# Kernel optimization log

Measured on AMD Instinct MI355X. Metric: run time of the kernel, lower is better.

Reference implementation:

```python
import jax, jax.numpy as jnp
import numpy as np

NUM_HEADS = 16


def setup_inputs() -> dict:
    key = jax.random.key(0)
    ks = jax.random.split(key, 6)
    B, N, M, C = 2, 2048, 2048, 1024
    return {
        "reference_data": jax.random.normal(ks[0], (B, N, C), dtype=jnp.float32),
        "target_data": jax.random.normal(ks[1], (B, M, C), dtype=jnp.float32),
        "Wq": jax.random.normal(ks[2], (C, C), dtype=jnp.float32) * (C ** -0.5),
        "Wkv": jax.random.normal(ks[3], (C, 2 * C), dtype=jnp.float32) * (C ** -0.5),
        "Wproj": jax.random.normal(ks[4], (C, C), dtype=jnp.float32) * (C ** -0.5),
        "bproj": jnp.zeros((C,), dtype=jnp.float32),
    }


def reference(reference_data, target_data, Wq, Wkv, Wproj, bproj):
    B, N, C = reference_data.shape
    M = target_data.shape[1]
    H = NUM_HEADS
    hd = C // H
    scale = hd ** -0.5
    # k, v from reference: [B, N, 2, H, hd] -> two [B, H, N, hd]
    kv = (reference_data @ Wkv).reshape(B, N, 2, H, hd)
    k = jnp.transpose(kv[:, :, 0], (0, 2, 1, 3))  # [B,H,N,hd]
    v = jnp.transpose(kv[:, :, 1], (0, 2, 1, 3))  # [B,H,N,hd]
    # q from target: [B, H, M, hd]
    q = jnp.transpose((target_data @ Wq).reshape(B, M, H, hd), (0, 2, 1, 3))
    attn = jnp.einsum("bhid,bhjd->bhij", q, k) * scale  # [B,H,M,N]
    attn = jax.nn.softmax(attn, axis=-1)
    x = jnp.einsum("bhij,bhjd->bhid", attn, v)  # [B,H,M,hd]
    x = jnp.transpose(x, (0, 2, 1, 3)).reshape(B, M, C)
    return x @ Wproj + bproj
```

## Files before the change

### kernel.cpp

```cpp
#include <hip/hip_runtime.h>
#include <hip/hip_bf16.h>
#include <stdint.h>

#define SEQ   2048
#define CH    1024
#define NH    16
#define HD    64

typedef short bf8 __attribute__((ext_vector_type(8)));
typedef short bf4 __attribute__((ext_vector_type(4)));
typedef float f4  __attribute__((ext_vector_type(4)));
typedef unsigned short u16;

#define GAS(p) ((const __attribute__((address_space(1))) void*)(p))
#define LAS(p) ((__attribute__((address_space(3))) void*)(p))

__device__ __forceinline__ u16 f2bf(float f) {
  uint32_t u = __float_as_uint(f);
  u += 0x7fffu + ((u >> 16) & 1u);
  return (u16)(u >> 16);
}

__device__ __forceinline__ uint32_t pk2bf(float a, float b) {
  float2 f; f.x = a; f.y = b;
  __hip_bfloat162 h = __float22bfloat162_rn(f);
  union { __hip_bfloat162 h; uint32_t u; } cv; cv.h = h;
  return cv.u;
}

__device__ __forceinline__ f4 MFMA32(bf8 a, bf8 b, f4 c) {
  return __builtin_amdgcn_mfma_f32_16x16x32_bf16(a, b, c, 0, 0, 0);
}

__device__ __forceinline__ f4 MFMA16(bf4 a, bf4 b, f4 c) {
#if __has_builtin(__builtin_amdgcn_mfma_f32_16x16x16_bf16)
  return __builtin_amdgcn_mfma_f32_16x16x16_bf16(a, b, c, 0, 0, 0);
#elif __has_builtin(__builtin_amdgcn_mfma_f32_16x16x16bf16_1k)
  return __builtin_amdgcn_mfma_f32_16x16x16bf16_1k(a, b, c, 0, 0, 0);
#else
  f4 d = c;
  asm volatile("v_mfma_f32_16x16x16_bf16 %0, %1, %2, %0"
               : "+v"(d) : "v"(a), "v"(b));
  return d;
#endif
}

__global__ void cvt2_bf16(const float* __restrict__ a, u16* __restrict__ oa,
                          const float* __restrict__ b, u16* __restrict__ ob) {
  int blk = blockIdx.x;
  const float* in; u16* out;
  if (blk < 4096) { in = a; out = oa; } else { in = b; out = ob; blk -= 4096; }
  int i = (blk * 256 + threadIdx.x) * 4;
  float4 f = *reinterpret_cast<const float4*>(in + i);
  ushort4 o;
  o.x = f2bf(f.x); o.y = f2bf(f.y); o.z = f2bf(f.z); o.w = f2bf(f.w);
  *reinterpret_cast<ushort4*>(out + i) = o;
}

__global__ void transp_all(const float* __restrict__ Wq, u16* __restrict__ Wqt,
                           const float* __restrict__ Wkv, u16* __restrict__ Wkvt,
                           const float* __restrict__ Wp, u16* __restrict__ Wpt) {
  __shared__ float tile[32][33];
  int x = blockIdx.x;
  const float* in; u16* out; int N;
  if (x < 32)       { in = Wq;  out = Wqt;  N = CH;     }
  else if (x < 96)  { in = Wkv; out = Wkvt; N = 2 * CH; x -= 32; }
  else              { in = Wp;  out = Wpt;  N = CH;     x -= 96; }
  const int K = CH;
  int bn = x * 32, bk = blockIdx.y * 32;
  int tx = threadIdx.x, ty = threadIdx.y;
  #pragma unroll
  for (int i = ty; i < 32; i += 8)
    tile[i][tx] = in[(size_t)(bk + i) * N + bn + tx];
  __syncthreads();
  #pragma unroll
  for (int i = ty; i < 32; i += 8)
    out[(size_t)(bn + i) * K + bk + tx] = f2bf(tile[tx][i]);
}

__global__ __launch_bounds__(256, 2)
void gemm_qkv(const u16* __restrict__ tgtb, const u16* __restrict__ refb,
              const u16* __restrict__ Wqt, const u16* __restrict__ Wkvt,
              u16* __restrict__ qb, u16* __restrict__ karr, u16* __restrict__ varr)
{
  __shared__ __align__(16) u16 As[128 * 32];
  __shared__ __align__(16) u16 Bs[128 * 32];
  const int tid = threadIdx.x;
  const int lane = tid & 63, wave = tid >> 6;
  const int l16 = lane & 15, q = lane >> 4;
  const bool isQ = blockIdx.x >= 16;
  const u16* A  = isQ ? tgtb : refb;
  const u16* Bt = isQ ? Wqt : Wkvt;
  const int n0 = (isQ ? (blockIdx.x - 16) : blockIdx.x) * 128;
  const int m0 = blockIdx.y * 128;
  const int wm = (wave >> 1) * 64, wn = (wave & 1) * 64;
  const int Kdim = CH;

  f4 acc[4][4] = {};

  for (int k0 = 0; k0 < Kdim; k0 += 32) {
    __syncthreads();
    {
      const int c = tid, c2 = tid + 256;
      __builtin_amdgcn_global_load_lds(
          GAS(&A[(size_t)(m0 + (c >> 2)) * Kdim + k0 + ((c & 3) << 3)]),
          LAS(&As[c << 3]), 16, 0, 0);
      __builtin_amdgcn_global_load_lds(
          GAS(&A[(size_t)(m0 + (c2 >> 2)) * Kdim + k0 + ((c2 & 3) << 3)]),
          LAS(&As[c2 << 3]), 16, 0, 0);
      __builtin_amdgcn_global_load_lds(
          GAS(&Bt[(size_t)(n0 + (c >> 2)) * Kdim + k0 + ((c & 3) << 3)]),
          LAS(&Bs[c << 3]), 16, 0, 0);
      __builtin_amdgcn_global_load_lds(
          GAS(&Bt[(size_t)(n0 + (c2 >> 2)) * Kdim + k0 + ((c2 & 3) << 3)]),
          LAS(&Bs[c2 << 3]), 16, 0, 0);
    }
    __syncthreads();
    bf8 a[4], b[4];
    #pragma unroll
    for (int i = 0; i < 4; ++i)
      a[i] = *reinterpret_cast<const bf8*>(&As[(wm + i * 16 + l16) * 32 + q * 8]);
    #pragma unroll
    for (int j = 0; j < 4; ++j)
      b[j] = *reinterpret_cast<const bf8*>(&Bs[(wn + j * 16 + l16) * 32 + q * 8]);
    #pragma unroll
    for (int i = 0; i < 4; ++i)
      #pragma unroll
      for (int j = 0; j < 4; ++j)
        acc[i][j] = MFMA32(a[i], b[j], acc[i][j]);
  }

  #pragma unroll
  for (int i = 0; i < 4; ++i) {
    const int mbase = m0 + wm + i * 16 + q * 4;
    #pragma unroll
    for (int j = 0; j < 4; ++j) {
      const int n = n0 + wn + j * 16 + l16;
      #pragma unroll
      for (int r = 0; r < 4; ++r) {
        const int m = mbase + r;
        float v = acc[i][j][r];
        if (isQ) {
          int b = m >> 11, ms = m & (SEQ - 1), h = n >> 6, d = n & 63;
          qb[(size_t)((b * NH + h) * SEQ + ms) * HD + d] = f2bf(v * 0.1803368801f);
        } else {
          int b = m >> 11, ns = m & (SEQ - 1);
          if (n < CH) {
            int h = n >> 6, d = n & 63;
            size_t base = (size_t)(b * NH + h) * SEQ * HD;
            int off = (((ns >> 4) * 2 + (d >> 5)) * 4 + ((d >> 3) & 3)) * 128
                      + (ns & 15) * 8 + (d & 7);
            karr[base + off] = f2bf(v);
          } else {
            int c2 = n - CH, h = c2 >> 6, d = c2 & 63;
            size_t base = (size_t)(b * NH + h) * SEQ * HD;
            int off = (((ns >> 4) * 4 + (d >> 4)) * 4 + ((ns >> 2) & 3)) * 64
                      + (d & 15) * 4 + (ns & 3);
            varr[base + off] = f2bf(v);
          }
        }
      }
    }
  }
}

__global__ __launch_bounds__(256, 2)
void gemm_proj(const u16* __restrict__ A, const u16* __restrict__ Bt,
               float* __restrict__ fo, const float* __restrict__ bias)
{
  __shared__ __align__(16) u16 As[128 * 32];
  __shared__ __align__(16) u16 Bs[128 * 32];
  const int tid = threadIdx.x;
  const int lane = tid & 63, wave = tid >> 6;
  const int l16 = lane & 15, q = lane >> 4;
  const int m0 = blockIdx.y * 128, n0 = blockIdx.x * 128;
  const int wm = (wave >> 1) * 64, wn = (wave & 1) * 64;
  const int Kdim = CH;

  f4 acc[4][4] = {};

  for (int k0 = 0; k0 < Kdim; k0 += 32) {
    __syncthreads();
    {
      const int c = tid, c2 = tid + 256;
      __builtin_amdgcn_global_load_lds(
          GAS(&A[(size_t)(m0 + (c >> 2)) * Kdim + k0 + ((c & 3) << 3)]),
          LAS(&As[c << 3]), 16, 0, 0);
      __builtin_amdgcn_global_load_lds(
          GAS(&A[(size_t)(m0 + (c2 >> 2)) * Kdim + k0 + ((c2 & 3) << 3)]),
          LAS(&As[c2 << 3]), 16, 0, 0);
      __builtin_amdgcn_global_load_lds(
          GAS(&Bt[(size_t)(n0 + (c >> 2)) * Kdim + k0 + ((c & 3) << 3)]),
          LAS(&Bs[c << 3]), 16, 0, 0);
      __builtin_amdgcn_global_load_lds(
          GAS(&Bt[(size_t)(n0 + (c2 >> 2)) * Kdim + k0 + ((c2 & 3) << 3)]),
          LAS(&Bs[c2 << 3]), 16, 0, 0);
    }
    __syncthreads();
    bf8 a[4], b[4];
    #pragma unroll
    for (int i = 0; i < 4; ++i)
      a[i] = *reinterpret_cast<const bf8*>(&As[(wm + i * 16 + l16) * 32 + q * 8]);
    #pragma unroll
    for (int j = 0; j < 4; ++j)
      b[j] = *reinterpret_cast<const bf8*>(&Bs[(wn + j * 16 + l16) * 32 + q * 8]);
    #pragma unroll
    for (int i = 0; i < 4; ++i)
      #pragma unroll
      for (int j = 0; j < 4; ++j)
        acc[i][j] = MFMA32(a[i], b[j], acc[i][j]);
  }

  #pragma unroll
  for (int i = 0; i < 4; ++i) {
    const int mbase = m0 + wm + i * 16 + q * 4;
    #pragma unroll
    for (int j = 0; j < 4; ++j) {
      const int n = n0 + wn + j * 16 + l16;
      #pragma unroll
      for (int r = 0; r < 4; ++r)
        fo[(size_t)(mbase + r) * CH + n] = acc[i][j][r] + bias[n];
    }
  }
}

__global__ __launch_bounds__(512, 4)
void attn(const u16* __restrict__ Q, const u16* __restrict__ Karr,
          const u16* __restrict__ Varr, u16* __restrict__ X)
{
  __shared__ __align__(16) u16 Ks[8192];
  __shared__ __align__(16) u16 Vs[8192];
  const int tid = threadIdx.x;
  const int lane = tid & 63, wave = tid >> 6;
  const int l16 = lane & 15, q = lane >> 4;
  const int bh = blockIdx.y;
  const int m0 = blockIdx.x * 128;
  const int wm = wave * 16;

  const u16* Qb = Q    + (size_t)bh * SEQ * HD;
  const u16* Kb = Karr + (size_t)bh * SEQ * HD;
  const u16* Vb = Varr + (size_t)bh * SEQ * HD;

  bf8 qf[2];
  #pragma unroll
  for (int ks = 0; ks < 2; ++ks)
    qf[ks] = *reinterpret_cast<const bf8*>(
        &Qb[(size_t)(m0 + wm + l16) * HD + ks * 32 + q * 8]);

  f4 o[4] = {};
  f4 lsum = {};

  for (int nt = 0; nt < SEQ; nt += 128) {
    __syncthreads();
    {
      const u16* kg = Kb + (size_t)(nt >> 4) * 1024;
      const u16* vg = Vb + (size_t)(nt >> 4) * 1024;
      #pragma unroll
      for (int s = 0; s < 2; ++s) {
        int c = tid + s * 512;
        __builtin_amdgcn_global_load_lds(GAS(kg + c * 8), LAS(Ks + c * 8), 16, 0, 0);
        __builtin_amdgcn_global_load_lds(GAS(vg + c * 8), LAS(Vs + c * 8), 16, 0, 0);
      }
    }
    __syncthreads();

    bf4 pa[8];
    #pragma unroll
    for (int j = 0; j < 8; ++j) {
      bf8 kf0 = *reinterpret_cast<const bf8*>(&Ks[((j * 2 + 0) * 4 + q) * 128 + l16 * 8]);
      bf8 kf1 = *reinterpret_cast<const bf8*>(&Ks[((j * 2 + 1) * 4 + q) * 128 + l16 * 8]);
      f4 z = {};
      z = MFMA32(kf0, qf[0], z);
      z = MFMA32(kf1, qf[1], z);
      f4 p;
      #pragma unroll
      for (int r = 0; r < 4; ++r) p[r] = exp2f(z[r]);
      lsum += p;
      union { bf4 v; uint32_t u[2]; } w;
      w.u[0] = pk2bf(p[0], p[1]);
      w.u[1] = pk2bf(p[2], p[3]);
      pa[j] = w.v;
    }

    #pragma unroll
    for (int j = 0; j < 8; ++j)
      #pragma unroll
      for (int dt = 0; dt < 4; ++dt) {
        bf4 vf = *reinterpret_cast<const bf4*>(&Vs[((j * 4 + dt) * 4 + q) * 64 + l16 * 4]);
        o[dt] = MFMA16(pa[j], vf, o[dt]);
      }
  }

  float ls = lsum[0] + lsum[1] + lsum[2] + lsum[3];
  ls += __shfl_xor(ls, 16);
  ls += __shfl_xor(ls, 32);
  float inv = 1.0f / ls;

  const int b = bh >> 4, h = bh & (NH - 1);
  #pragma unroll
  for (int r = 0; r < 4; ++r) {
    float ir = __shfl(inv, q * 4 + r);
    int m = m0 + wm + q * 4 + r;
    #pragma unroll
    for (int dt = 0; dt < 4; ++dt) {
      int d = dt * 16 + l16;
      X[(size_t)(b * SEQ + m) * CH + h * HD + d] = f2bf(o[dt][r] * ir);
    }
  }
}

extern "C" void kernel_launch(void* const* d_in, const int* in_sizes, int n_in,
                              void* d_out, int out_size, void* d_ws, size_t ws_size,
                              hipStream_t stream) {
  const float* ref   = (const float*)d_in[0];
  const float* tgt   = (const float*)d_in[1];
  const float* Wq    = (const float*)d_in[2];
  const float* Wkv   = (const float*)d_in[3];
  const float* Wproj = (const float*)d_in[4];
  const float* bproj = (const float*)d_in[5];
  float* out = (float*)d_out;

  char* ws = (char*)d_ws;
  u16* refb = (u16*)(ws);
  u16* tgtb = (u16*)(ws + (8  << 20));
  u16* Wqt  = (u16*)(ws + (16 << 20));
  u16* Wkvt = (u16*)(ws + (18 << 20));
  u16* Wpt  = (u16*)(ws + (22 << 20));
  u16* qb   = (u16*)(ws + (24 << 20));
  u16* karr = (u16*)(ws + (32 << 20));
  u16* varr = (u16*)(ws + (40 << 20));
  u16* xb   = (u16*)(ws + (48 << 20));

  cvt2_bf16<<<8192, 256, 0, stream>>>(ref, refb, tgt, tgtb);
  transp_all<<<dim3(128, 32), dim3(32, 8), 0, stream>>>(Wq, Wqt, Wkv, Wkvt, Wproj, Wpt);

  gemm_qkv<<<dim3(24, 32), 256, 0, stream>>>(tgtb, refb, Wqt, Wkvt, qb, karr, varr);

  attn<<<dim3(16, 32), 512, 0, stream>>>(qb, karr, varr, xb);

  gemm_proj<<<dim3(8, 32), 256, 0, stream>>>(xb, Wpt, out, bproj);
}
```

Before: 228.2 us.

## Double-buffer LDS tiles in GEMMs and attention, compute row sums via MFMA

Measured after the change: 222.9 us. 2.3% less time.

```diff
diff --git a/kernel.cpp b/kernel.cpp
--- a/kernel.cpp
+++ b/kernel.cpp
@@ -83,8 +83,8 @@
               const u16* __restrict__ Wqt, const u16* __restrict__ Wkvt,
               u16* __restrict__ qb, u16* __restrict__ karr, u16* __restrict__ varr)
 {
-  __shared__ __align__(16) u16 As[128 * 32];
-  __shared__ __align__(16) u16 Bs[128 * 32];
+  __shared__ __align__(16) u16 As[2][4096];
+  __shared__ __align__(16) u16 Bs[2][4096];
   const int tid = threadIdx.x;
   const int lane = tid & 63, wave = tid >> 6;
   const int l16 = lane & 15, q = lane >> 4;
@@ -95,70 +95,76 @@
   const int m0 = blockIdx.y * 128;
   const int wm = (wave >> 1) * 64, wn = (wave & 1) * 64;
   const int Kdim = CH;
+  const int c = tid, c2 = tid + 256;
+  const int ar = c >> 2, ac = (c & 3) << 3, ar2 = c2 >> 2, ac2 = (c2 & 3) << 3;
 
   f4 acc[4][4] = {};
 
-  for (int k0 = 0; k0 < Kdim; k0 += 32) {
+  #define STAGE_G(buf, k0)                                                      \
+    { __builtin_amdgcn_global_load_lds(                                         \
+          GAS(&A[(size_t)(m0 + ar) * Kdim + (k0) + ac]),                        \
+          LAS(&As[buf][c << 3]), 16, 0, 0);                                     \
+      __builtin_amdgcn_global_load_lds(                                         \
+          GAS(&A[(size_t)(m0 + ar2) * Kdim + (k0) + ac2]),                      \
+          LAS(&As[buf][c2 << 3]), 16, 0, 0);                                    \
+      __builtin_amdgcn_global_load_lds(                                         \
+          GAS(&Bt[(size_t)(n0 + ar) * Kdim + (k0) + ac]),                       \
+          LAS(&Bs[buf][c << 3]), 16, 0, 0);                                     \
+      __builtin_amdgcn_global_load_lds(                                         \
+          GAS(&Bt[(size_t)(n0 + ar2) * Kdim + (k0) + ac2]),                     \
+          LAS(&Bs[buf][c2 << 3]), 16, 0, 0); }
+
+  STAGE_G(0, 0);
+  for (int kk = 0; kk < 32; ++kk) {
     __syncthreads();
-    {
-      const int c = tid, c2 = tid + 256;
-      __builtin_amdgcn_global_load_lds(
-          GAS(&A[(size_t)(m0 + (c >> 2)) * Kdim + k0 + ((c & 3) << 3)]),
-          LAS(&As[c << 3]), 16, 0, 0);
-      __builtin_amdgcn_global_load_lds(
-          GAS(&A[(size_t)(m0 + (c2 >> 2)) * Kdim + k0 + ((c2 & 3) << 3)]),
-          LAS(&As[c2 << 3]), 16, 0, 0);
-      __builtin_amdgcn_global_load_lds(
-          GAS(&Bt[(size_t)(n0 + (c >> 2)) * Kdim + k0 + ((c & 3) << 3)]),
-          LAS(&Bs[c << 3]), 16, 0, 0);
-      __builtin_amdgcn_global_load_lds(
-          GAS(&Bt[(size_t)(n0 + (c2 >> 2)) * Kdim + k0 + ((c2 & 3) << 3)]),
-          LAS(&Bs[c2 << 3]), 16, 0, 0);
-    }
-    __syncthreads();
+    if (kk < 31) STAGE_G((kk + 1) & 1, (kk + 1) * 32);
+    const u16* as = As[kk & 1];
+    const u16* bs = Bs[kk & 1];
     bf8 a[4], b[4];
     #pragma unroll
     for (int i = 0; i < 4; ++i)
-      a[i] = *reinterpret_cast<const bf8*>(&As[(wm + i * 16 + l16) * 32 + q * 8]);
+      a[i] = *reinterpret_cast<const bf8*>(&as[(wm + i * 16 + l16) * 32 + q * 8]);
     #pragma unroll
     for (int j = 0; j < 4; ++j)
-      b[j] = *reinterpret_cast<const bf8*>(&Bs[(wn + j * 16 + l16) * 32 + q * 8]);
+      b[j] = *reinterpret_cast<const bf8*>(&bs[(wn + j * 16 + l16) * 32 + q * 8]);
     #pragma unroll
     for (int i = 0; i < 4; ++i)
       #pragma unroll
       for (int j = 0; j < 4; ++j)
         acc[i][j] = MFMA32(a[i], b[j], acc[i][j]);
   }
+  #undef STAGE_G
 
   #pragma unroll
   for (int i = 0; i < 4; ++i) {
     const int mbase = m0 + wm + i * 16 + q * 4;
+    const int b = mbase >> 11, ns0 = mbase & (SEQ - 1);
     #pragma unroll
     for (int j = 0; j < 4; ++j) {
       const int n = n0 + wn + j * 16 + l16;
-      #pragma unroll
-      for (int r = 0; r < 4; ++r) {
-        const int m = mbase + r;
-        float v = acc[i][j][r];
-        if (isQ) {
-          int b = m >> 11, ms = m & (SEQ - 1), h = n >> 6, d = n & 63;
-          qb[(size_t)((b * NH + h) * SEQ + ms) * HD + d] = f2bf(v * 0.1803368801f);
-        } else {
-          int b = m >> 11, ns = m & (SEQ - 1);
-          if (n < CH) {
-            int h = n >> 6, d = n & 63;
-            size_t base = (size_t)(b * NH + h) * SEQ * HD;
-            int off = (((ns >> 4) * 2 + (d >> 5)) * 4 + ((d >> 3) & 3)) * 128
-                      + (ns & 15) * 8 + (d & 7);
-            karr[base + off] = f2bf(v);
-          } else {
-            int c2 = n - CH, h = c2 >> 6, d = c2 & 63;
-            size_t base = (size_t)(b * NH + h) * SEQ * HD;
-            int off = (((ns >> 4) * 4 + (d >> 4)) * 4 + ((ns >> 2) & 3)) * 64
-                      + (d & 15) * 4 + (ns & 3);
-            varr[base + off] = f2bf(v);
-          }
-        }
+      if (isQ) {
+        int h = n >> 6, d = n & 63;
+        #pragma unroll
+        for (int r = 0; r < 4; ++r)
+          qb[(size_t)((b * NH + h) * SEQ + ns0 + r) * HD + d] =
+              f2bf(acc[i][j][r] * 0.1803368801f);
+      } else if (n < CH) {
+        int h = n >> 6, d = n & 63;
+        size_t base = (size_t)(b * NH + h) * SEQ * HD;
+        int off = (((ns0 >> 4) * 2 + (d >> 5)) * 4 + ((d >> 3) & 3)) * 128
+                  + (d & 7);
+        #pragma unroll
+        for (int r = 0; r < 4; ++r)
+          karr[base + off + ((ns0 + r) & 15) * 8] = f2bf(acc[i][j][r]);
+      } else {
+        int c2v = n - CH, h = c2v >> 6, d = c2v & 63;
+        size_t base = (size_t)(b * NH + h) * SEQ * HD;
+        int off = (((ns0 >> 4) * 4 + (d >> 4)) * 4 + ((ns0 >> 2) & 3)) * 64
+                  + (d & 15) * 4;
+        ushort4 st;
+        st.x = f2bf(acc[i][j][0]); st.y = f2bf(acc[i][j][1]);
+        st.z = f2bf(acc[i][j][2]); st.w = f2bf(acc[i][j][3]);
+        *reinterpret_cast<ushort4*>(&varr[base + off]) = st;
       }
     }
   }
@@ -168,48 +174,53 @@
 void gemm_proj(const u16* __restrict__ A, const u16* __restrict__ Bt,
                float* __restrict__ fo, const float* __restrict__ bias)
 {
-  __shared__ __align__(16) u16 As[128 * 32];
-  __shared__ __align__(16) u16 Bs[128 * 32];
+  __shared__ __align__(16) u16 As[2][4096];
+  __shared__ __align__(16) u16 Bs[2][4096];
   const int tid = threadIdx.x;
   const int lane = tid & 63, wave = tid >> 6;
   const int l16 = lane & 15, q = lane >> 4;
   const int m0 = blockIdx.y * 128, n0 = blockIdx.x * 128;
   const int wm = (wave >> 1) * 64, wn = (wave & 1) * 64;
   const int Kdim = CH;
+  const int c = tid, c2 = tid + 256;
+  const int ar = c >> 2, ac = (c & 3) << 3, ar2 = c2 >> 2, ac2 = (c2 & 3) << 3;
 
   f4 acc[4][4] = {};
 
-  for (int k0 = 0; k0 < Kdim; k0 += 32) {
+  #define STAGE_P(buf, k0)                                                      \
+    { __builtin_amdgcn_global_load_lds(                                         \
+          GAS(&A[(size_t)(m0 + ar) * Kdim + (k0) + ac]),                        \
+          LAS(&As[buf][c << 3]), 16, 0, 0);                                     \
+      __builtin_amdgcn_global_load_lds(                                         \
+          GAS(&A[(size_t)(m0 + ar2) * Kdim + (k0) + ac2]),                      \
+          LAS(&As[buf][c2 << 3]), 16, 0, 0);                                    \
+      __builtin_amdgcn_global_load_lds(                                         \
+          GAS(&Bt[(size_t)(n0 + ar) * Kdim + (k0) + ac]),                       \
+          LAS(&Bs[buf][c << 3]), 16, 0, 0);                                     \
+      __builtin_amdgcn_global_load_lds(                                         \
+          GAS(&Bt[(size_t)(n0 + ar2) * Kdim + (k0) + ac2]),                     \
+          LAS(&Bs[buf][c2 << 3]), 16, 0, 0); }
+
+  STAGE_P(0, 0);
+  for (int kk = 0; kk < 32; ++kk) {
     __syncthreads();
-    {
-      const int c = tid, c2 = tid + 256;
-      __builtin_amdgcn_global_load_lds(
-          GAS(&A[(size_t)(m0 + (c >> 2)) * Kdim + k0 + ((c & 3) << 3)]),
-          LAS(&As[c << 3]), 16, 0, 0);
-      __builtin_amdgcn_global_load_lds(
-          GAS(&A[(size_t)(m0 + (c2 >> 2)) * Kdim + k0 + ((c2 & 3) << 3)]),
-          LAS(&As[c2 << 3]), 16, 0, 0);
-      __builtin_amdgcn_global_load_lds(
-          GAS(&Bt[(size_t)(n0 + (c >> 2)) * Kdim + k0 + ((c & 3) << 3)]),
-          LAS(&Bs[c << 3]), 16, 0, 0);
-      __builtin_amdgcn_global_load_lds(
-          GAS(&Bt[(size_t)(n0 + (c2 >> 2)) * Kdim + k0 + ((c2 & 3) << 3)]),
-          LAS(&Bs[c2 << 3]), 16, 0, 0);
-    }
-    __syncthreads();
+    if (kk < 31) STAGE_P((kk + 1) & 1, (kk + 1) * 32);
+    const u16* as = As[kk & 1];
+    const u16* bs = Bs[kk & 1];
     bf8 a[4], b[4];
     #pragma unroll
     for (int i = 0; i < 4; ++i)
-      a[i] = *reinterpret_cast<const bf8*>(&As[(wm + i * 16 + l16) * 32 + q * 8]);
+      a[i] = *reinterpret_cast<const bf8*>(&as[(wm + i * 16 + l16) * 32 + q * 8]);
     #pragma unroll
     for (int j = 0; j < 4; ++j)
-      b[j] = *reinterpret_cast<const bf8*>(&Bs[(wn + j * 16 + l16) * 32 + q * 8]);
+      b[j] = *reinterpret_cast<const bf8*>(&bs[(wn + j * 16 + l16) * 32 + q * 8]);
     #pragma unroll
     for (int i = 0; i < 4; ++i)
       #pragma unroll
       for (int j = 0; j < 4; ++j)
         acc[i][j] = MFMA32(a[i], b[j], acc[i][j]);
   }
+  #undef STAGE_P
 
   #pragma unroll
   for (int i = 0; i < 4; ++i) {
@@ -228,14 +239,14 @@
 void attn(const u16* __restrict__ Q, const u16* __restrict__ Karr,
           const u16* __restrict__ Varr, u16* __restrict__ X)
 {
-  __shared__ __align__(16) u16 Ks[8192];
-  __shared__ __align__(16) u16 Vs[8192];
+  __shared__ __align__(16) u16 Ks[2][8192];
+  __shared__ __align__(16) u16 Vs[2][8192];
   const int tid = threadIdx.x;
-  const int lane = tid & 63, wave = tid >> 6;
+  const int lane = tid & 63;
   const int l16 = lane & 15, q = lane >> 4;
   const int bh = blockIdx.y;
   const int m0 = blockIdx.x * 128;
-  const int wm = wave * 16;
+  const int wm = (tid >> 6) * 16;
 
   const u16* Qb = Q    + (size_t)bh * SEQ * HD;
   const u16* Kb = Karr + (size_t)bh * SEQ * HD;
@@ -247,59 +258,61 @@
     qf[ks] = *reinterpret_cast<const bf8*>(
         &Qb[(size_t)(m0 + wm + l16) * HD + ks * 32 + q * 8]);
 
+  const short one_bf = 0x3F80;
+  const bf4 ones = {one_bf, one_bf, one_bf, one_bf};
+
   f4 o[4] = {};
-  f4 lsum = {};
-
-  for (int nt = 0; nt < SEQ; nt += 128) {
+  f4 ds = {};
+
+  #define STAGE_A(buf, t)                                                       \
+    { const u16* kg = Kb + (size_t)(t) * 8192;                                  \
+      const u16* vg = Vb + (size_t)(t) * 8192;                                  \
+      _Pragma("unroll")                                                         \
+      for (int s = 0; s < 2; ++s) {                                             \
+        int cc = tid + s * 512;                                                 \
+        __builtin_amdgcn_global_load_lds(GAS(kg + cc * 8),                      \
+                                         LAS(&Ks[buf][cc * 8]), 16, 0, 0);      \
+        __builtin_amdgcn_global_load_lds(GAS(vg + cc * 8),                      \
+                                         LAS(&Vs[buf][cc * 8]), 16, 0, 0);      \
+      } }
+
+  STAGE_A(0, 0);
+  for (int t = 0; t < SEQ / 128; ++t) {
     __syncthreads();
-    {
-      const u16* kg = Kb + (size_t)(nt >> 4) * 1024;
-      const u16* vg = Vb + (size_t)(nt >> 4) * 1024;
-      #pragma unroll
-      for (int s = 0; s < 2; ++s) {
-        int c = tid + s * 512;
-        __builtin_amdgcn_global_load_lds(GAS(kg + c * 8), LAS(Ks + c * 8), 16, 0, 0);
-        __builtin_amdgcn_global_load_lds(GAS(vg + c * 8), LAS(Vs + c * 8), 16, 0, 0);
-      }
-    }
-    __syncthreads();
+    if (t < SEQ / 128 - 1) STAGE_A((t + 1) & 1, t + 1);
+    const u16* ks = Ks[t & 1];
+    const u16* vs = Vs[t & 1];
 
     bf4 pa[8];
     #pragma unroll
     for (int j = 0; j < 8; ++j) {
-      bf8 kf0 = *reinterpret_cast<const bf8*>(&Ks[((j * 2 + 0) * 4 + q) * 128 + l16 * 8]);
-      bf8 kf1 = *reinterpret_cast<const bf8*>(&Ks[((j * 2 + 1) * 4 + q) * 128 + l16 * 8]);
+      bf8 kf0 = *reinterpret_cast<const bf8*>(&ks[((j * 2 + 0) * 4 + q) * 128 + l16 * 8]);
+      bf8 kf1 = *reinterpret_cast<const bf8*>(&ks[((j * 2 + 1) * 4 + q) * 128 + l16 * 8]);
       f4 z = {};
       z = MFMA32(kf0, qf[0], z);
       z = MFMA32(kf1, qf[1], z);
-      f4 p;
-      #pragma unroll
-      for (int r = 0; r < 4; ++r) p[r] = exp2f(z[r]);
-      lsum += p;
       union { bf4 v; uint32_t u[2]; } w;
-      w.u[0] = pk2bf(p[0], p[1]);
-      w.u[1] = pk2bf(p[2], p[3]);
+      w.u[0] = pk2bf(exp2f(z[0]), exp2f(z[1]));
+      w.u[1] = pk2bf(exp2f(z[2]), exp2f(z[3]));
       pa[j] = w.v;
     }
 
     #pragma unroll
-    for (int j = 0; j < 8; ++j)
+    for (int j = 0; j < 8; ++j) {
+      ds = MFMA16(pa[j], ones, ds);
       #pragma unroll
       for (int dt = 0; dt < 4; ++dt) {
-        bf4 vf = *reinterpret_cast<const bf4*>(&Vs[((j * 4 + dt) * 4 + q) * 64 + l16 * 4]);
+        bf4 vf = *reinterpret_cast<const bf4*>(&vs[((j * 4 + dt) * 4 + q) * 64 + l16 * 4]);
         o[dt] = MFMA16(pa[j], vf, o[dt]);
       }
-  }
-
-  float ls = lsum[0] + lsum[1] + lsum[2] + lsum[3];
-  ls += __shfl_xor(ls, 16);
-  ls += __shfl_xor(ls, 32);
-  float inv = 1.0f / ls;
+    }
+  }
+  #undef STAGE_A
 
   const int b = bh >> 4, h = bh & (NH - 1);
   #pragma unroll
   for (int r = 0; r < 4; ++r) {
-    float ir = __shfl(inv, q * 4 + r);
+    float ir = 1.0f / ds[r];
     int m = m0 + wm + q * 4 + r;
     #pragma unroll
     for (int dt = 0; dt < 4; ++dt) {
```
